# Kernel tuning notes

Hardware: AMD Instinct MI355X
Metric: run time of the kernel (lower is better)

## Reference

```python
import jax, jax.numpy as jnp
import numpy as np

B, C, T, H, W = 1, 512, 4, 64, 64
GROUPS = 32
EPS = 1e-6


def group_norm(x, gamma, beta):
    # torch GroupNorm on 5D input normalizes over (C/G, T, H, W) per group
    b, c, t, h, w = x.shape
    xg = x.reshape(b, GROUPS, c // GROUPS, t, h, w)
    mu = xg.mean(axis=(2, 3, 4, 5), keepdims=True)
    var = xg.var(axis=(2, 3, 4, 5), keepdims=True)
    xn = ((xg - mu) * jax.lax.rsqrt(var + EPS)).reshape(b, c, t, h, w)
    return xn * gamma[None, :, None, None, None] + beta[None, :, None, None, None]


def setup_inputs() -> dict:
    key = jax.random.key(0)
    ks = jax.random.split(key, 10)
    s = 0.02
    return {
        "x": jax.random.normal(ks[0], (B, C, T, H, W), dtype=jnp.float32),
        "gamma": jnp.ones((C,), dtype=jnp.float32),
        "beta": jnp.zeros((C,), dtype=jnp.float32),
        "wq": jax.random.normal(ks[1], (C, C), dtype=jnp.float32) * s,
        "bq": jnp.zeros((C,), dtype=jnp.float32),
        "wk": jax.random.normal(ks[2], (C, C), dtype=jnp.float32) * s,
        "bk": jnp.zeros((C,), dtype=jnp.float32),
        "wv": jax.random.normal(ks[3], (C, C), dtype=jnp.float32) * s,
        "bv": jnp.zeros((C,), dtype=jnp.float32),
        "wp": jax.random.normal(ks[4], (C, C), dtype=jnp.float32) * s,
        "bp": jnp.zeros((C,), dtype=jnp.float32),
    }


def reference(x, gamma, beta, wq, bq, wk, bk, wv, bv, wp, bp):
    b, c, t, h, w = x.shape
    n = h * w
    hn = group_norm(x, gamma, beta)
    # fold time into batch: (b t) c (h w)
    hn = hn.transpose(0, 2, 1, 3, 4).reshape(b * t, c, n)
    # 1x1 convs == channel matmuls
    q = jnp.einsum('oc,bcn->bno', wq, hn) + bq            # (bt, n, c)
    k = jnp.einsum('oc,bcn->bon', wk, hn) + bk[:, None]   # (bt, c, n)
    v = jnp.einsum('oc,bcn->bon', wv, hn) + bv[:, None]   # (bt, c, n)
    scale = float(c) ** -0.5
    attn = jax.nn.softmax(jnp.einsum('bic,bcj->bij', q * scale, k), axis=-1)  # (bt, n, n)
    out = jnp.einsum('bcj,bij->bci', v, attn)             # (bt, c, n)
    out = jnp.einsum('oc,bcn->bon', wp, out) + bp[:, None]
    out = out.reshape(b, t, c, h, w).transpose(0, 2, 1, 3, 4)
    return x + out
```

## Files before the change

### kernel.cpp

```cpp
#include <hip/hip_runtime.h>
#include <hip/hip_bf16.h>

typedef __attribute__((ext_vector_type(8))) short short8;
typedef __attribute__((ext_vector_type(4))) short short4v;
typedef __attribute__((ext_vector_type(4))) float f32x4;

__device__ __forceinline__ short f2bf(float f) {
  __hip_bfloat16 h = __float2bfloat16(f);
  return *reinterpret_cast<short*>(&h);
}
__device__ __forceinline__ float bf2f(short s) {
  return __uint_as_float(((unsigned)(unsigned short)s) << 16);
}
__device__ __forceinline__ void glds16(const short* src, short* dst) {
  __builtin_amdgcn_global_load_lds(
      (const __attribute__((address_space(1))) unsigned int*)src,
      (__attribute__((address_space(3))) unsigned int*)dst, 16, 0, 0);
}
__device__ __forceinline__ float wave_red_sum(float v) {
  for (int i = 1; i < 64; i <<= 1) v += __shfl_xor(v, i);
  return v;
}

__global__ __launch_bounds__(256) void pre_a(const float* __restrict__ w0, short* __restrict__ o0,
                                             const float* __restrict__ w1, short* __restrict__ o1,
                                             const float* __restrict__ w2, short* __restrict__ o2,
                                             const float* __restrict__ w3, short* __restrict__ o3,
                                             const float* __restrict__ x, float* __restrict__ part) {
  int b = blockIdx.x;
  if (b < 1024) {
    int which = b >> 8;
    const float* w = (which == 0) ? w0 : (which == 1) ? w1 : (which == 2) ? w2 : w3;
    short* o       = (which == 0) ? o0 : (which == 1) ? o1 : (which == 2) ? o2 : o3;
    int i = (b & 255) * 256 + threadIdx.x;
    float4 v = ((const float4*)w)[i];
    short4v r;
    r.x = f2bf(v.x); r.y = f2bf(v.y); r.z = f2bf(v.z); r.w = f2bf(v.w);
    *(short4v*)&o[i*4] = r;
    return;
  }
  int u = b - 1024;
  int g = u & 31, s = u >> 5;
  const float4* base = (const float4*)(x + (size_t)g * 262144 + (size_t)s * 32768);
  float sum = 0.f, sq = 0.f;
  for (int i = threadIdx.x; i < 8192; i += 256) {
    float4 v = base[i];
    sum += v.x + v.y + v.z + v.w;
    sq  += v.x*v.x + v.y*v.y + v.z*v.z + v.w*v.w;
  }
  sum = wave_red_sum(sum); sq = wave_red_sum(sq);
  __shared__ float ls[4], lq[4];
  int w = threadIdx.x >> 6, lane = threadIdx.x & 63;
  if (lane == 0) { ls[w] = sum; lq[w] = sq; }
  __syncthreads();
  if (threadIdx.x == 0) {
    part[(g*8 + s)*2 + 0] = ls[0]+ls[1]+ls[2]+ls[3];
    part[(g*8 + s)*2 + 1] = lq[0]+lq[1]+lq[2]+lq[3];
  }
}

__global__ __launch_bounds__(256) void pre_b(const short* __restrict__ in, short* __restrict__ out,
                                             const float* __restrict__ part, float* __restrict__ stats,
                                             const float* __restrict__ wp, const float* __restrict__ bv,
                                             float* __restrict__ bpv) {
  __shared__ short T[64 * 72];
  int b = blockIdx.x;
  int tid = threadIdx.x;
  if (b < 64) {
    int c0 = (b & 7) * 64, i0 = (b >> 3) * 64;
#pragma unroll
    for (int it = 0; it < 2; ++it) {
      int u = it * 256 + tid;
      int r = u >> 3, k8 = (u & 7) * 8;
      *(short8*)&T[r * 72 + k8] = *(const short8*)&in[(size_t)(c0 + r) * 512 + i0 + k8];
    }
    __syncthreads();
#pragma unroll
    for (int it = 0; it < 2; ++it) {
      int u = it * 256 + tid;
      int c = u & 63, tg = u >> 6;
      short8 o;
#pragma unroll
      for (int j = 0; j < 8; ++j) o[j] = T[(tg * 8 + j) * 72 + c];
      *(short8*)&out[(size_t)(i0 + c) * 512 + c0 + tg * 8] = o;
    }
    return;
  }
  if (b == 64) {
    int g = tid;
    if (g < 32) {
      float s1 = 0.f, s2 = 0.f;
      for (int s = 0; s < 8; ++s) { s1 += part[(g*8+s)*2]; s2 += part[(g*8+s)*2+1]; }
      float mean = s1 * (1.f/262144.f);
      float var  = s2 * (1.f/262144.f) - mean*mean;
      stats[g]      = mean;
      stats[32 + g] = rsqrtf(var + 1e-6f);
    }
    return;
  }
  int o = (b - 65) * 256 + tid;
  float s = 0.f;
  for (int c = 0; c < 512; ++c) s += wp[(size_t)o * 512 + c] * bv[c];
  bpv[o] = s;
}

enum { G_QKVW = 0, G_S = 1, G_PVT = 2, G_WPV = 3 };

template<int MODE, int NKT>
__global__ __launch_bounds__(512, 4) void gemm256(
    const short* __restrict__ A, const short* __restrict__ B0,
    const short* __restrict__ B1, const short* __restrict__ B2,
    short* __restrict__ out0, short* __restrict__ outT,
    const float* __restrict__ bias0, const float* __restrict__ bias1, const float* __restrict__ bias2,
    float* __restrict__ spart, float scale0,
    int lda, int ldb) {
  const int tid  = threadIdx.x;
  const int d    = blockIdx.x;

  if (MODE == G_WPV && d >= 8) {
    int u = d - 8;
    int n  = (u & 7) * 512 + tid;
    int c0 = ((u >> 3) & 63) * 8;
    int t  = u >> 9;
    const float* xx = (const float*)B1;
    short8 o8;
#pragma unroll
    for (int j = 0; j < 8; ++j) {
      int c = c0 + j, g = c >> 4;
      float v  = xx[(size_t)c * 16384 + t * 4096 + n];
      float hv = (v - bias0[g]) * bias0[32 + g] * bias1[c] + bias2[c];
      o8[j] = f2bf(hv);
    }
    *(short8*)&outT[((size_t)t * 4096 + n) * 512 + c0] = o8;
    return;
  }
  if (MODE == G_PVT && d >= 512) {
    int row = (d - 512) * 512 + tid;
    const f32x4* p = (const f32x4*)(spart + (size_t)row * 32);
    float s = 0.f;
#pragma unroll
    for (int i = 0; i < 4; ++i) { f32x4 v = p[i]; s += v[0] + v[1] + v[2] + v[3]; }
    const_cast<float*>(bias0)[row] = 1.f / s;
    return;
  }

  const int lane = tid & 63;
  const int w    = tid >> 6;
  const int wr   = w >> 2;
  const int wc   = w & 3;

  int bm_b, bn_b, z = 0, tt = 0;
  if (MODE == G_QKVW) {
    int xcd = d & 7, sl_ = d >> 3;
    bn_b = sl_ & 1; bm_b = xcd * 16 + ((sl_ >> 1) & 15); z = sl_ >> 5;
  } else if (MODE == G_S) {
    int xcd = d & 7, sl_ = d >> 3;
    bm_b = xcd * 4 + (sl_ & 3); bn_b = (sl_ >> 2) & 15; tt = sl_ >> 6;
  } else if (MODE == G_PVT) {
    int xcd = d & 7, sl_ = d >> 3;
    bm_b = xcd * 4 + (sl_ & 3); bn_b = (sl_ >> 2) & 1; z = (sl_ >> 3) & 1; tt = sl_ >> 4;
  } else {
    bm_b = d & 3; bn_b = d >> 2;
  }
  const int bm0 = bm_b * 128;
  const int bn0 = bn_b * 256;

  const short* Abase = A;
  const short* Bt = B0;
  const float* bias = bias0;
  float scale = 1.f;
  int ktile0 = 0;
  if (MODE == G_QKVW) {
    Bt    = (z == 0) ? B0 : (z == 1) ? B1 : B2;
    bias  = (z == 0) ? bias0 : (z == 1) ? bias1 : bias2;
    scale = (z == 0) ? scale0 : 1.f;
  }
  if (MODE == G_S) {
    Abase = A  + (size_t)tt * 2097152;
    Bt    = B0 + (size_t)tt * 2097152;
  }
  if (MODE == G_PVT) {
    Abase  = A  + (size_t)tt * 16777216;
    Bt     = B0 + (size_t)tt * 4096;
    ktile0 = z * NKT;
  }

  __shared__ __align__(16) short Ls[36864];

  const int r0 = tid >> 2, s0 = tid & 3;
  const int srcoff = ((s0 - (r0 >> 1)) & 3) << 3;
  const short* Asrc = Abase + (size_t)(bm0 + r0) * lda + ktile0 * 32 + srcoff;
  const short* Bsrc = Bt    + (size_t)(bn0 + r0) * ldb + ktile0 * 32 + srcoff;
  const size_t offB128 = (size_t)128 * ldb;

  auto stage = [&](int kt, int b) {
    short* As = Ls + b * 12288;
    short* Bs = As + 4096;
    int kc = kt * 32;
    glds16(Asrc + kc,           As + tid * 8);
    glds16(Bsrc + kc,           Bs + tid * 8);
    glds16(Bsrc + kc + offB128, Bs + 4096 + tid * 8);
  };

  const int lr = lane & 15, sl = lane >> 4;
  int aoff[4], boff[4];
#pragma unroll
  for (int i = 0; i < 4; ++i) {
    int ra = wr * 64 + i * 16 + lr;
    aoff[i] = ra * 32 + (((sl + (ra >> 1)) & 3) << 3);
    int rb = wc * 64 + i * 16 + lr;
    boff[i] = 4096 + rb * 32 + (((sl + (rb >> 1)) & 3) << 3);
  }

  f32x4 acc[4][4] = {};

  stage(0, 0);
  stage(1, 1);
  asm volatile("s_waitcnt vmcnt(3)" ::: "memory");
  asm volatile("s_barrier" ::: "memory");

  int bcur = 0;
  for (int t = 0; t < NKT; ++t) {
    int b2 = bcur + 2; if (b2 >= 3) b2 -= 3;
    if (t + 2 < NKT) stage(t + 2, b2);
    const short* As = Ls + bcur * 12288;
    short8 af[4], bf8[4];
#pragma unroll
    for (int i = 0; i < 4; ++i) af[i] = *(const short8*)&As[aoff[i]];
#pragma unroll
    for (int i = 0; i < 4; ++i) bf8[i] = *(const short8*)&As[boff[i]];
    __builtin_amdgcn_s_setprio(1);
#pragma unroll
    for (int mi = 0; mi < 4; ++mi)
#pragma unroll
      for (int ni = 0; ni < 4; ++ni)
        acc[mi][ni] = __builtin_amdgcn_mfma_f32_16x16x32_bf16(af[mi], bf8[ni], acc[mi][ni], 0, 0, 0);
    __builtin_amdgcn_s_setprio(0);
    if (t + 2 < NKT)        { asm volatile("s_waitcnt vmcnt(3)" ::: "memory"); }
    else if (t == NKT - 2)  { asm volatile("s_waitcnt vmcnt(0)" ::: "memory"); }
    asm volatile("s_barrier" ::: "memory");
    bcur = (bcur == 2) ? 0 : bcur + 1;
  }

  if ((MODE == G_PVT) || (MODE == G_QKVW && z == 2)) {
#pragma unroll
    for (int ni = 0; ni < 4; ++ni) {
      int brow = wc * 64 + ni * 16 + lr;
      float badd = (MODE == G_QKVW) ? bias[bn0 + brow] : 0.f;
#pragma unroll
      for (int mi = 0; mi < 4; ++mi) {
        int bcol0 = wr * 64 + mi * 16 + sl * 4;
        short4v pk;
#pragma unroll
        for (int r = 0; r < 4; ++r) pk[r] = f2bf(acc[mi][ni][r] + badd);
        *(short4v*)&Ls[brow * 132 + bcol0] = pk;
      }
    }
    __syncthreads();
#pragma unroll
    for (int it = 0; it < 8; ++it) {
      int u = it * 512 + tid;
      int ol = u >> 4, c8 = (u & 15) * 8;
      short8 v = *(const short8*)&Ls[ol * 132 + c8];
      if (MODE == G_PVT)
        *(short8*)&out0[((size_t)(tt * 2 + z) * 512 + bn0 + ol) * 4096 + bm0 + c8] = v;
      else
        *(short8*)&outT[(size_t)(bn0 + ol) * 16384 + bm0 + c8] = v;
    }
  } else {
#pragma unroll
    for (int mi = 0; mi < 4; ++mi) {
      int row0 = wr * 64 + mi * 16 + sl * 4;
#pragma unroll
      for (int ni = 0; ni < 4; ++ni) {
        int col = wc * 64 + ni * 16 + lr;
        float badd = (MODE == G_QKVW) ? bias[bn0 + col] : 0.f;
#pragma unroll
        for (int r = 0; r < 4; ++r) {
          float v = acc[mi][ni][r];
          if (MODE == G_QKVW) v = (v + badd) * scale;
          if (MODE == G_S)    v = __expf(v);
          Ls[(row0 + r) * 264 + col] = f2bf(v);
        }
      }
    }
    __syncthreads();
#pragma unroll
    for (int it = 0; it < 8; ++it) {
      int u = it * 512 + tid;
      int rl = u >> 5, c8 = (u & 31) * 8;
      short8 v = *(const short8*)&Ls[rl * 264 + c8];
      int grow = bm0 + rl;
      if (MODE == G_QKVW)
        *(short8*)&out0[(size_t)z * 16384 * 512 + (size_t)grow * 512 + bn0 + c8] = v;
      else if (MODE == G_S)
        *(short8*)&out0[(size_t)tt * 16777216 + (size_t)grow * 4096 + bn0 + c8] = v;
      else
        *(short8*)&out0[(size_t)grow * 512 + bn0 + c8] = v;
      if (MODE == G_S) {
        float s = 0.f;
#pragma unroll
        for (int j = 0; j < 8; ++j) s += bf2f(v[j]);
        s += __shfl_xor(s, 1); s += __shfl_xor(s, 2); s += __shfl_xor(s, 4);
        s += __shfl_xor(s, 8); s += __shfl_xor(s, 16);
        if ((lane & 31) == 0) spart[((size_t)tt * 4096 + grow) * 32 + bn_b] = s;
      }
    }
  }
}

__global__ __launch_bounds__(256) void reduce_pv(const short* __restrict__ PVp,
                                                 const float* __restrict__ rinv,
                                                 const float* __restrict__ x,
                                                 float* __restrict__ out) {
  int b = blockIdx.x;
  int t = b >> 11;
  int gid = (b & 2047) * 256 + threadIdx.x;
  int o = gid >> 10, n = (gid & 1023) * 4;
  size_t oi = (size_t)o * 16384 + t * 4096 + n;
  const short* P  = PVp + (size_t)t * 4194304;
  const float* rv = rinv + (size_t)t * 4096;
  float4 xr = *(const float4*)&x[oi];
  float4 rr = *(const float4*)&rv[n];
  float s0 = 0.f, s1 = 0.f, s2 = 0.f, s3 = 0.f;
#pragma unroll
  for (int sp = 0; sp < 2; ++sp) {
    short4v v = *(const short4v*)&P[((size_t)sp * 512 + o) * 4096 + n];
    s0 += bf2f(v.x); s1 += bf2f(v.y); s2 += bf2f(v.z); s3 += bf2f(v.w);
  }
  float4 og;
  og.x = xr.x + s0 * rr.x;
  og.y = xr.y + s1 * rr.y;
  og.z = xr.z + s2 * rr.z;
  og.w = xr.w + s3 * rr.w;
  *(float4*)&out[oi] = og;
}

extern "C" void kernel_launch(void* const* d_in, const int* in_sizes, int n_in,
                              void* d_out, int out_size, void* d_ws, size_t ws_size,
                              hipStream_t stream) {
  const float* x     = (const float*)d_in[0];
  const float* gamma = (const float*)d_in[1];
  const float* beta  = (const float*)d_in[2];
  const float* wq    = (const float*)d_in[3];
  const float* bq    = (const float*)d_in[4];
  const float* wk    = (const float*)d_in[5];
  const float* bk    = (const float*)d_in[6];
  const float* wv    = (const float*)d_in[7];
  const float* bv    = (const float*)d_in[8];
  const float* wp    = (const float*)d_in[9];
  const float* bp    = (const float*)d_in[10];

  char* ws = (char*)d_ws;
  size_t off = 0;
  auto alloc = [&](size_t bytes) -> void* {
    void* p = ws + off;
    off += (bytes + 255) & ~(size_t)255;
    return p;
  };
  short* SP   = (short*)alloc((size_t)4 * 4096 * 4096 * 2);
  short* HnT  = SP;
  short* QK   = (short*)alloc((size_t)2 * 16384 * 512 * 2);
  short* VWT  = (short*)alloc((size_t)512 * 16384 * 2);
  short* PVp  = (short*)alloc((size_t)4 * 2 * 512 * 4096 * 2);
  short* WqB  = (short*)alloc((size_t)512 * 512 * 2);
  short* WkB  = (short*)alloc((size_t)512 * 512 * 2);
  short* WvB  = (short*)alloc((size_t)512 * 512 * 2);
  short* WpB  = (short*)alloc((size_t)512 * 512 * 2);
  short* WvT  = (short*)alloc((size_t)512 * 512 * 2);
  short* WpvB = (short*)alloc((size_t)512 * 512 * 2);
  float* spart= (float*)alloc((size_t)16384 * 32 * 4);
  float* rinv = (float*)alloc((size_t)16384 * 4);
  float* bpv  = (float*)alloc((size_t)512 * 4);
  float* part = (float*)alloc(32 * 8 * 2 * 4);
  float* stats= (float*)alloc(64 * 4);
  if (off > ws_size) return;

  const float scale = 0.044194173824159216f;

  pre_a<<<1280, 256, 0, stream>>>(wq, WqB, wk, WkB, wv, WvB, wp, WpB, x, part);
  pre_b<<<67, 256, 0, stream>>>(WvB, WvT, part, stats, wp, bv, bpv);
  gemm256<G_WPV, 16><<<2056, 512, 0, stream>>>(
      WpB, WvT, (const short*)x, nullptr, WpvB, HnT, stats, gamma, beta, nullptr, 1.f, 512, 512);

  gemm256<G_QKVW, 16><<<768, 512, 0, stream>>>(
      HnT, WqB, WkB, WpvB, QK, VWT, bq, bk, bpv, nullptr, scale, 512, 512);

  gemm256<G_S, 16><<<2048, 512, 0, stream>>>(
      QK, QK + (size_t)16384 * 512, nullptr, nullptr, SP, nullptr, nullptr, nullptr, nullptr, spart,
      1.f, 512, 512);
  gemm256<G_PVT, 64><<<544, 512, 0, stream>>>(
      SP, VWT, nullptr, nullptr, PVp, nullptr, rinv, nullptr, nullptr, spart, 1.f, 4096, 16384);
  reduce_pv<<<8192, 256, 0, stream>>>(PVp, rinv, x, (float*)d_out);
}
```

Before: 248.3 us.

## Enlarge S-GEMM tile to 256x256 with 1024-thread blocks

The QK^T score GEMM now uses 1024-thread blocks computing 256x256 output tiles instead of 512-thread blocks on 128x256 tiles. The grid is halved and the block-index mapping is adjusted to match. Shared memory grows to about 132 KB, and each thread issues two global-to-LDS loads per stage instead of three. The intent is more operand reuse per byte loaded and fewer blocks to schedule, at the cost of one block per CU and lower occupancy for hiding latency.

```diff
diff --git a/kernel.cpp b/kernel.cpp
--- a/kernel.cpp
+++ b/kernel.cpp
@@ -107,13 +107,21 @@
 enum { G_QKVW = 0, G_S = 1, G_PVT = 2, G_WPV = 3 };
 
 template<int MODE, int NKT>
-__global__ __launch_bounds__(512, 4) void gemm256(
+__global__ __launch_bounds__(MODE == G_S ? 1024 : 512, MODE == G_S ? 1 : 4)
+void gemm256(
     const short* __restrict__ A, const short* __restrict__ B0,
     const short* __restrict__ B1, const short* __restrict__ B2,
     short* __restrict__ out0, short* __restrict__ outT,
     const float* __restrict__ bias0, const float* __restrict__ bias1, const float* __restrict__ bias2,
     float* __restrict__ spart, float scale0,
     int lda, int ldb) {
+  constexpr int THREADS = (MODE == G_S) ? 1024 : 512;
+  constexpr int BM      = (MODE == G_S) ? 256 : 128;
+  constexpr int AR32    = BM * 32;
+  constexpr int BUFSZ   = (BM + 256) * 32;
+  constexpr int LSSZ    = (MODE == G_S) ? 67584 : 36864;
+  constexpr int NVM     = (MODE == G_S) ? 2 : 3;
+
   const int tid  = threadIdx.x;
   const int d    = blockIdx.x;
 
@@ -155,14 +163,14 @@
     bn_b = sl_ & 1; bm_b = xcd * 16 + ((sl_ >> 1) & 15); z = sl_ >> 5;
   } else if (MODE == G_S) {
     int xcd = d & 7, sl_ = d >> 3;
-    bm_b = xcd * 4 + (sl_ & 3); bn_b = (sl_ >> 2) & 15; tt = sl_ >> 6;
+    bm_b = xcd * 2 + (sl_ & 1); bn_b = (sl_ >> 1) & 15; tt = sl_ >> 5;
   } else if (MODE == G_PVT) {
     int xcd = d & 7, sl_ = d >> 3;
     bm_b = xcd * 4 + (sl_ & 3); bn_b = (sl_ >> 2) & 1; z = (sl_ >> 3) & 1; tt = sl_ >> 4;
   } else {
     bm_b = d & 3; bn_b = d >> 2;
   }
-  const int bm0 = bm_b * 128;
+  const int bm0 = bm_b * BM;
   const int bn0 = bn_b * 256;
 
   const short* Abase = A;
@@ -185,7 +193,7 @@
     ktile0 = z * NKT;
   }
 
-  __shared__ __align__(16) short Ls[36864];
+  __shared__ __align__(16) short Ls[LSSZ];
 
   const int r0 = tid >> 2, s0 = tid & 3;
   const int srcoff = ((s0 - (r0 >> 1)) & 3) << 3;
@@ -194,12 +202,17 @@
   const size_t offB128 = (size_t)128 * ldb;
 
   auto stage = [&](int kt, int b) {
-    short* As = Ls + b * 12288;
-    short* Bs = As + 4096;
+    short* As = Ls + b * BUFSZ;
+    short* Bs = As + AR32;
     int kc = kt * 32;
-    glds16(Asrc + kc,           As + tid * 8);
-    glds16(Bsrc + kc,           Bs + tid * 8);
-    glds16(Bsrc + kc + offB128, Bs + 4096 + tid * 8);
+    if (MODE == G_S) {
+      glds16(Asrc + kc, As + tid * 8);
+      glds16(Bsrc + kc, Bs + tid * 8);
+    } else {
+      glds16(Asrc + kc,           As + tid * 8);
+      glds16(Bsrc + kc,           Bs + tid * 8);
+      glds16(Bsrc + kc + offB128, Bs + 4096 + tid * 8);
+    }
   };
 
   const int lr = lane & 15, sl = lane >> 4;
@@ -209,21 +222,21 @@
     int ra = wr * 64 + i * 16 + lr;
     aoff[i] = ra * 32 + (((sl + (ra >> 1)) & 3) << 3);
     int rb = wc * 64 + i * 16 + lr;
-    boff[i] = 4096 + rb * 32 + (((sl + (rb >> 1)) & 3) << 3);
+    boff[i] = AR32 + rb * 32 + (((sl + (rb >> 1)) & 3) << 3);
   }
 
   f32x4 acc[4][4] = {};
 
   stage(0, 0);
   stage(1, 1);
-  asm volatile("s_waitcnt vmcnt(3)" ::: "memory");
+  asm volatile("s_waitcnt vmcnt(%0)" :: "i"(NVM) : "memory");
   asm volatile("s_barrier" ::: "memory");
 
   int bcur = 0;
   for (int t = 0; t < NKT; ++t) {
     int b2 = bcur + 2; if (b2 >= 3) b2 -= 3;
     if (t + 2 < NKT) stage(t + 2, b2);
-    const short* As = Ls + bcur * 12288;
+    const short* As = Ls + bcur * BUFSZ;
     short8 af[4], bf8[4];
 #pragma unroll
     for (int i = 0; i < 4; ++i) af[i] = *(const short8*)&As[aoff[i]];
@@ -236,7 +249,7 @@
       for (int ni = 0; ni < 4; ++ni)
         acc[mi][ni] = __builtin_amdgcn_mfma_f32_16x16x32_bf16(af[mi], bf8[ni], acc[mi][ni], 0, 0, 0);
     __builtin_amdgcn_s_setprio(0);
-    if (t + 2 < NKT)        { asm volatile("s_waitcnt vmcnt(3)" ::: "memory"); }
+    if (t + 2 < NKT)        { asm volatile("s_waitcnt vmcnt(%0)" :: "i"(NVM) : "memory"); }
     else if (t == NKT - 2)  { asm volatile("s_waitcnt vmcnt(0)" ::: "memory"); }
     asm volatile("s_barrier" ::: "memory");
     bcur = (bcur == 2) ? 0 : bcur + 1;
@@ -259,7 +272,7 @@
     __syncthreads();
 #pragma unroll
     for (int it = 0; it < 8; ++it) {
-      int u = it * 512 + tid;
+      int u = it * THREADS + tid;
       int ol = u >> 4, c8 = (u & 15) * 8;
       short8 v = *(const short8*)&Ls[ol * 132 + c8];
       if (MODE == G_PVT)
@@ -287,7 +300,7 @@
     __syncthreads();
 #pragma unroll
     for (int it = 0; it < 8; ++it) {
-      int u = it * 512 + tid;
+      int u = it * THREADS + tid;
       int rl = u >> 5, c8 = (u & 31) * 8;
       short8 v = *(const short8*)&Ls[rl * 264 + c8];
       int grow = bm0 + rl;
@@ -386,7 +399,7 @@
   gemm256<G_QKVW, 16><<<768, 512, 0, stream>>>(
       HnT, WqB, WkB, WpvB, QK, VWT, bq, bk, bpv, nullptr, scale, 512, 512);
 
-  gemm256<G_S, 16><<<2048, 512, 0, stream>>>(
+  gemm256<G_S, 16><<<1024, 1024, 0, stream>>>(
       QK, QK + (size_t)16384 * 512, nullptr, nullptr, SP, nullptr, nullptr, nullptr, nullptr, spart,
       1.f, 512, 512);
   gemm256<G_PVT, 64><<<544, 512, 0, stream>>>(
```

Result: slower. 266.2 us (+7.2%).
